# Performance work log

Measured on AMD Instinct MI355X. Metric: run time of the kernel, lower is better.

The kernel has to match this reference:

```python
import math
import jax, jax.numpy as jnp
import numpy as np

NQ, NK = 4096, 8192
D_Q, D_K, D_ATTN, H, D_OUT = 256, 256, 64, 4, 256


def setup_inputs() -> dict:
    key = jax.random.key(0)
    ks = jax.random.split(key, 10)
    s = 0.02
    return {
        "x_Q": jax.random.normal(ks[0], (NQ, D_Q), jnp.float32),
        "x_K": jax.random.normal(ks[1], (NK, D_K), jnp.float32),
        "mask": jax.random.randint(ks[2], (NQ, NK), 0, 2, jnp.int32),
        # per-head projection weights, stored as (H, in, out) so y = x @ W
        "Wq": jax.random.normal(ks[3], (H, D_Q, D_ATTN), jnp.float32) * s,
        "Wk": jax.random.normal(ks[4], (H, D_K, D_ATTN), jnp.float32) * s,
        "Wv": jax.random.normal(ks[5], (H, D_K, D_ATTN), jnp.float32) * s,
        # per-head gate: Linear(d_Q, 1) + sigmoid
        "Wg": jax.random.normal(ks[6], (H, D_Q), jnp.float32) * s,
        "bg": jax.random.normal(ks[7], (H,), jnp.float32) * s,
        # output projection Linear(d_attn, d_out) with bias
        "Wo": jax.random.normal(ks[8], (D_ATTN, D_OUT), jnp.float32) * s,
        "bo": jax.random.normal(ks[9], (D_OUT,), jnp.float32) * s,
    }


def reference(x_Q, x_K, mask, Wq, Wk, Wv, Wg, bg, Wo, bo):
    m = mask.astype(x_Q.dtype)  # (NQ, NK) 0/1
    # Stacked per-head projections (original loops over heads)
    Q = jnp.einsum("nq,hqa->hna", x_Q, Wq)  # (H, NQ, A)
    K = jnp.einsum("mk,hka->hma", x_K, Wk)  # (H, NK, A)
    V = jnp.einsum("mk,hka->hma", x_K, Wv)  # (H, NK, A)
    scale = 1.0 / math.sqrt(D_ATTN)
    scores = jnp.einsum("hna,hma->hnm", Q, K) * scale  # (H, NQ, NK)
    # masked_softmax: (mask * x).masked_fill(mask == 0, -inf) then softmax over keys
    X = jnp.where(m == 0, -jnp.inf, m * scores)
    attn = jax.nn.softmax(X, axis=-1)
    heads = jnp.einsum("hnm,hma->hna", attn, V)  # (H, NQ, A)
    gates = jax.nn.sigmoid(jnp.einsum("nq,hq->hn", x_Q, Wg) + bg[:, None])  # (H, NQ)
    combined = jnp.einsum("hna,hn->na", heads, gates)  # (NQ, A)
    return combined @ Wo + bo  # (NQ, D_OUT)
```

## Files before the change

### kernel.cpp

```cpp
#include <hip/hip_runtime.h>
#include <hip/hip_bf16.h>

#define NQ 4096
#define NK 8192
#define DQK 256
#define DA 64
#define NH 4
#define DOUT 256
#define KSPLIT 16
#define KLEN (NK / KSPLIT)
#define NQT (NQ / 32)
#define LOG2E 1.44269504088896340736f
#define QSCALE (0.125f * LOG2E)

typedef __attribute__((ext_vector_type(8))) short bf16x8;
typedef __attribute__((ext_vector_type(4))) float f32x4;
typedef __attribute__((ext_vector_type(4))) _Float16 f16x4;

__device__ inline unsigned short f2bf(float f) {
  union { float f; unsigned u; } v; v.f = f;
  unsigned r = v.u + 0x7fff + ((v.u >> 16) & 1);
  return (unsigned short)(r >> 16);
}

__device__ inline unsigned pk2(float a, float b) {
  float2 t; t.x = a; t.y = b;
  __hip_bfloat162 r = __float22bfloat162_rn(t);
  return *(unsigned*)&r;
}

__global__ __launch_bounds__(256) void maskbits_kernel(
    const int* __restrict__ mask, unsigned long long* __restrict__ bits64) {
  const int NW = 8192 * 4;
  int wid = blockIdx.x * 4 + (threadIdx.x >> 6);
  int lane = threadIdx.x & 63;
  for (int j = 0; j < 2; ++j) {
    int v[8];
#pragma unroll
    for (int u = 0; u < 8; ++u) {
      int c = wid + (j * 8 + u) * NW;
      v[u] = mask[(size_t)(c >> 7) * NK + (c & 127) * 64 + lane];
    }
#pragma unroll
    for (int u = 0; u < 8; ++u) {
      unsigned long long b = __ballot(v[u] != 0);
      int c = wid + (j * 8 + u) * NW;
      if (lane == 0) bits64[c] = b;
    }
  }
}

__global__ __launch_bounds__(256) void proj_kernel(
    const float* __restrict__ xQ, const float* __restrict__ xK,
    const float* __restrict__ Wq, const float* __restrict__ Wk,
    const float* __restrict__ Wv,
    unsigned short* __restrict__ Qp, unsigned short* __restrict__ Kp,
    unsigned short* __restrict__ Vt) {
  __shared__ __align__(16) unsigned short Wt[64][264];

  int b = blockIdx.x;
  int proj, h, rb;
  if (b < 64)        { proj = 0; h = b >> 4;  rb = b & 15; }
  else if (b < 192)  { proj = 1; b -= 64;  h = b >> 5; rb = b & 31; }
  else               { proj = 2; b -= 192; h = b >> 5; rb = b & 31; }
  const float* x = (proj == 0) ? xQ : xK;
  const float* W = (proj == 0 ? Wq : (proj == 1 ? Wk : Wv)) + (size_t)h * 256 * 64;

  for (int i = threadIdx.x; i < 16384; i += 256)
    Wt[i & 63][i >> 6] = f2bf(W[i]);
  __syncthreads();

  int lane = threadIdx.x & 63, wv = threadIdx.x >> 6;
  int quad = lane >> 4, n16 = lane & 15;
  int r0 = rb * 256 + wv * 64;

  f32x4 acc[4][4];
#pragma unroll
  for (int mt = 0; mt < 4; ++mt)
#pragma unroll
    for (int nt = 0; nt < 4; ++nt)
      acc[mt][nt] = (f32x4){0.f, 0.f, 0.f, 0.f};

#pragma unroll
  for (int it = 0; it < 8; ++it) {
    const int k0 = it * 32;
    bf16x8 af[4];
#pragma unroll
    for (int mt = 0; mt < 4; ++mt) {
      const float* xp = x + (size_t)(r0 + mt * 16 + n16) * 256 + k0 + quad * 8;
      const float4 a0 = *(const float4*)xp;
      const float4 a1 = *(const float4*)(xp + 4);
      bf16x8 a;
      a[0] = (short)f2bf(a0.x); a[1] = (short)f2bf(a0.y);
      a[2] = (short)f2bf(a0.z); a[3] = (short)f2bf(a0.w);
      a[4] = (short)f2bf(a1.x); a[5] = (short)f2bf(a1.y);
      a[6] = (short)f2bf(a1.z); a[7] = (short)f2bf(a1.w);
      af[mt] = a;
    }
    bf16x8 bfr[4];
#pragma unroll
    for (int nt = 0; nt < 4; ++nt)
      bfr[nt] = *(const bf16x8*)&Wt[nt * 16 + n16][k0 + quad * 8];
#pragma unroll
    for (int mt = 0; mt < 4; ++mt)
#pragma unroll
      for (int nt = 0; nt < 4; ++nt)
        acc[mt][nt] = __builtin_amdgcn_mfma_f32_16x16x32_bf16(
            af[mt], bfr[nt], acc[mt][nt], 0, 0, 0);
  }

  if (proj < 2) {
    unsigned short* outp =
        (proj == 0 ? Qp : Kp) + (size_t)h * (size_t)(proj == 0 ? NQ : NK) * 64;
    const float sc = (proj == 0) ? QSCALE : 1.0f;
#pragma unroll
    for (int mt = 0; mt < 4; ++mt)
#pragma unroll
      for (int nt = 0; nt < 4; ++nt)
#pragma unroll
        for (int r = 0; r < 4; ++r) {
          int row = r0 + mt * 16 + quad * 4 + r;
          int col = nt * 16 + n16;
          outp[(size_t)row * 64 + col] = f2bf(acc[mt][nt][r] * sc);
        }
  } else {
    unsigned short* vtp = Vt + (size_t)h * 64 * NK;
#pragma unroll
    for (int mt = 0; mt < 4; ++mt)
#pragma unroll
      for (int nt = 0; nt < 4; ++nt) {
        int d = nt * 16 + n16;
        int key0 = r0 + mt * 16 + quad * 4;
        ushort4 pk;
        pk.x = f2bf(acc[mt][nt][0]); pk.y = f2bf(acc[mt][nt][1]);
        pk.z = f2bf(acc[mt][nt][2]); pk.w = f2bf(acc[mt][nt][3]);
        *(ushort4*)&vtp[(size_t)d * NK + key0] = pk;
      }
  }
}

__global__ __launch_bounds__(256) void attn_kernel(
    const unsigned short* __restrict__ Qp, const unsigned short* __restrict__ Kp,
    const unsigned short* __restrict__ Vt, const unsigned* __restrict__ bits,
    _Float16* __restrict__ Opart, float* __restrict__ Lpart) {
  __shared__ __align__(16) unsigned short Plds[4][2][32][40];

  int b = blockIdx.x;
  int ks = b & 15, h = (b >> 4) & 3, qg = b >> 6;
  int wv = threadIdx.x >> 6, lane = threadIdx.x & 63;
  int quad = lane >> 4, n16 = lane & 15;
  int qt = qg * 4 + wv;
  int qb = qt * 32;

  bf16x8 qf[2][2];
#pragma unroll
  for (int qc = 0; qc < 2; ++qc)
#pragma unroll
    for (int c = 0; c < 2; ++c)
      qf[qc][c] = *(const bf16x8*)&Qp[((size_t)h * NQ + qb + qc * 16 + n16) * 64 +
                                      c * 32 + quad * 8];

  bf16x8 onesA;
  {
    short v = (n16 == 0) ? (short)0x3F80 : (short)0;
#pragma unroll
    for (int i = 0; i < 8; ++i) onesA[i] = v;
  }

  f32x4 o[4][2];
#pragma unroll
  for (int dt = 0; dt < 4; ++dt)
#pragma unroll
    for (int qc = 0; qc < 2; ++qc) o[dt][qc] = (f32x4){0.f, 0.f, 0.f, 0.f};
  f32x4 l5[2];
  l5[0] = (f32x4){0.f, 0.f, 0.f, 0.f};
  l5[1] = (f32x4){0.f, 0.f, 0.f, 0.f};

  const unsigned short* Kptr =
      Kp + (size_t)h * NK * 64 + (size_t)(ks * KLEN + n16) * 64 + quad * 8;
  const unsigned short* Vptr =
      Vt + (size_t)h * 64 * NK + (size_t)n16 * NK + ks * KLEN + quad * 8;
  const unsigned* bq0 = bits + (size_t)(qb + n16) * (NK / 32) + ks * (KLEN / 32);
  const unsigned* bq1 = bits + (size_t)(qb + 16 + n16) * (NK / 32) + ks * (KLEN / 32);

  bf16x8 kf[2][2], vf[4];
#pragma unroll
  for (int kr = 0; kr < 2; ++kr)
#pragma unroll
    for (int c = 0; c < 2; ++c)
      kf[kr][c] = *(const bf16x8*)(Kptr + kr * 16 * 64 + c * 32);
#pragma unroll
  for (int dt = 0; dt < 4; ++dt)
    vf[dt] = *(const bf16x8*)(Vptr + (size_t)dt * 16 * NK);

#pragma unroll
  for (int kb = 0; kb < KLEN / 32; ++kb) {
    bf16x8 kn[2][2], vn[4];
    if (kb < KLEN / 32 - 1) {
      const unsigned short* Kn = Kptr + (size_t)(kb + 1) * 32 * 64;
      const unsigned short* Vn = Vptr + (kb + 1) * 32;
#pragma unroll
      for (int kr = 0; kr < 2; ++kr)
#pragma unroll
        for (int c = 0; c < 2; ++c)
          kn[kr][c] = *(const bf16x8*)(Kn + kr * 16 * 64 + c * 32);
#pragma unroll
      for (int dt = 0; dt < 4; ++dt)
        vn[dt] = *(const bf16x8*)(Vn + (size_t)dt * 16 * NK);
    }
    unsigned wqa0 = bq0[kb];
    unsigned wqa1 = bq1[kb];

    f32x4 s[2][2];
#pragma unroll
    for (int kr = 0; kr < 2; ++kr)
#pragma unroll
      for (int qc = 0; qc < 2; ++qc) {
        f32x4 acc = (f32x4){0.f, 0.f, 0.f, 0.f};
        acc = __builtin_amdgcn_mfma_f32_16x16x32_bf16(kf[kr][0], qf[qc][0], acc, 0, 0, 0);
        acc = __builtin_amdgcn_mfma_f32_16x16x32_bf16(kf[kr][1], qf[qc][1], acc, 0, 0, 0);
        s[kr][qc] = acc;
      }

    unsigned short* pbuf = &Plds[wv][kb & 1][0][0];
#pragma unroll
    for (int qc = 0; qc < 2; ++qc) {
      unsigned wq0 = (qc == 0 ? wqa0 : wqa1) >> (quad * 4);
      float e[8];
#pragma unroll
      for (int kr = 0; kr < 2; ++kr)
#pragma unroll
        for (int r = 0; r < 4; ++r) {
          float ev = __builtin_amdgcn_exp2f(s[kr][qc][r]);
          e[kr * 4 + r] = (wq0 & (1u << (kr * 16 + r))) ? ev : 0.f;
        }
      unsigned short* prow = pbuf + (qc * 16 + n16) * 40;
      uint2 w01, w23;
      w01.x = pk2(e[0], e[1]); w01.y = pk2(e[2], e[3]);
      w23.x = pk2(e[4], e[5]); w23.y = pk2(e[6], e[7]);
      *(uint2*)(prow + quad * 4) = w01;
      *(uint2*)(prow + 16 + quad * 4) = w23;
    }

    bf16x8 pb0 = *(const bf16x8*)(pbuf + n16 * 40 + quad * 8);
    bf16x8 pb1 = *(const bf16x8*)(pbuf + (16 + n16) * 40 + quad * 8);

#pragma unroll
    for (int dt = 0; dt < 4; ++dt) {
      o[dt][0] = __builtin_amdgcn_mfma_f32_16x16x32_bf16(vf[dt], pb0, o[dt][0], 0, 0, 0);
      o[dt][1] = __builtin_amdgcn_mfma_f32_16x16x32_bf16(vf[dt], pb1, o[dt][1], 0, 0, 0);
    }
    l5[0] = __builtin_amdgcn_mfma_f32_16x16x32_bf16(onesA, pb0, l5[0], 0, 0, 0);
    l5[1] = __builtin_amdgcn_mfma_f32_16x16x32_bf16(onesA, pb1, l5[1], 0, 0, 0);

    if (kb < KLEN / 32 - 1) {
#pragma unroll
      for (int kr = 0; kr < 2; ++kr)
#pragma unroll
        for (int c = 0; c < 2; ++c) kf[kr][c] = kn[kr][c];
#pragma unroll
      for (int dt = 0; dt < 4; ++dt) vf[dt] = vn[dt];
    }
  }

  const size_t tb = ((size_t)h * NQT + qt) * KSPLIT + ks;
#pragma unroll
  for (int qc = 0; qc < 2; ++qc) {
#pragma unroll
    for (int dt = 0; dt < 4; ++dt) {
      size_t idx = (tb * 32 + qc * 16 + n16) * 64 + dt * 16 + quad * 4;
      f16x4 ov;
      ov[0] = (_Float16)o[dt][qc][0]; ov[1] = (_Float16)o[dt][qc][1];
      ov[2] = (_Float16)o[dt][qc][2]; ov[3] = (_Float16)o[dt][qc][3];
      *(f16x4*)&Opart[idx] = ov;
    }
  }
  if (quad == 0) {
    Lpart[tb * 32 + n16] = l5[0][0];
    Lpart[tb * 32 + 16 + n16] = l5[1][0];
  }
}

__global__ __launch_bounds__(256) void combine_kernel(
    const _Float16* __restrict__ Opart, const float* __restrict__ Lpart,
    const float* __restrict__ xQ, const float* __restrict__ Wg,
    const float* __restrict__ bg, const float* __restrict__ Wo,
    const float* __restrict__ bo, float* __restrict__ out) {
  __shared__ float comb[16][64];
  __shared__ float gred[16][4][4];
  __shared__ float glds[16][4];
  int nb = blockIdx.x;
  int tid = threadIdx.x;

  {
    int r = tid >> 4, hh = (tid >> 2) & 3, c = tid & 3;
    const float* xp = xQ + (size_t)(nb * 16 + r) * 256 + c * 64;
    const float* wp = Wg + hh * 256 + c * 64;
    float s = 0.f;
#pragma unroll
    for (int e = 0; e < 64; ++e) s = fmaf(xp[e], wp[e], s);
    gred[r][hh][c] = s;
  }
  __syncthreads();
  if (tid < 64) {
    int r = tid >> 2, hh = tid & 3;
    float s = gred[r][hh][0] + gred[r][hh][1] + gred[r][hh][2] + gred[r][hh][3];
    glds[r][hh] = 1.f / (1.f + __expf(-(s + bg[hh])));
  }
  __syncthreads();

  int r4 = tid >> 6, a = tid & 63;
  int qt = nb >> 1, rbase = (nb & 1) * 16;

  for (int p = 0; p < 4; ++p) {
    int r = p * 4 + r4;
    int rl = rbase + r;
    float csum = 0.f;
#pragma unroll
    for (int h = 0; h < NH; ++h) {
      size_t t0 = ((size_t)h * NQT + qt) * KSPLIT;
      float accO = 0.f, lt = 0.f;
#pragma unroll
      for (int s = 0; s < KSPLIT; ++s) {
        size_t t = t0 + s;
        accO += (float)Opart[(t * 32 + rl) * 64 + a];
        lt += Lpart[t * 32 + rl];
      }
      csum += glds[r][h] * accO / lt;
    }
    comb[r][a] = csum;
  }
  __syncthreads();

  int j = tid;
  float accv[16];
#pragma unroll
  for (int r = 0; r < 16; ++r) accv[r] = bo[j];
  for (int aa = 0; aa < 64; ++aa) {
    float w = Wo[(size_t)aa * 256 + j];
#pragma unroll
    for (int r = 0; r < 16; ++r) accv[r] = fmaf(comb[r][aa], w, accv[r]);
  }
#pragma unroll
  for (int r = 0; r < 16; ++r)
    out[(size_t)(nb * 16 + r) * 256 + j] = accv[r];
}

extern "C" void kernel_launch(void* const* d_in, const int* in_sizes, int n_in,
                              void* d_out, int out_size, void* d_ws, size_t ws_size,
                              hipStream_t stream) {
  const float* xQ  = (const float*)d_in[0];
  const float* xK  = (const float*)d_in[1];
  const int*   mask= (const int*)d_in[2];
  const float* Wq  = (const float*)d_in[3];
  const float* Wk  = (const float*)d_in[4];
  const float* Wv  = (const float*)d_in[5];
  const float* Wg  = (const float*)d_in[6];
  const float* bg  = (const float*)d_in[7];
  const float* Wo  = (const float*)d_in[8];
  const float* bo  = (const float*)d_in[9];
  float* out = (float*)d_out;

  char* ws = (char*)d_ws;
  unsigned short* Qp   = (unsigned short*)(ws + 0);
  unsigned short* Kp   = (unsigned short*)(ws + 2097152);
  unsigned short* Vt   = (unsigned short*)(ws + 6291456);
  unsigned*       bits = (unsigned*)(ws + 10485760);
  float*          Lp   = (float*)(ws + 14745600);
  _Float16*       Op   = (_Float16*)(ws + 15794176);

  maskbits_kernel<<<dim3(8192), dim3(256), 0, stream>>>(
      mask, (unsigned long long*)bits);
  proj_kernel<<<dim3(320), dim3(256), 0, stream>>>(xQ, xK, Wq, Wk, Wv, Qp, Kp, Vt);
  attn_kernel<<<dim3(2048), dim3(256), 0, stream>>>(Qp, Kp, Vt, bits, Op, Lp);
  combine_kernel<<<dim3(NQ / 16), dim3(256), 0, stream>>>(Op, Lp, xQ, Wg, bg,
                                                          Wo, bo, out);
}
```

Measured before the change: 429.5 us.

## Keep softmax probabilities in registers using fp16 MFMA and halve key split

```diff
diff --git a/kernel.cpp b/kernel.cpp
--- a/kernel.cpp
+++ b/kernel.cpp
@@ -7,7 +7,7 @@
 #define DA 64
 #define NH 4
 #define DOUT 256
-#define KSPLIT 16
+#define KSPLIT 8
 #define KLEN (NK / KSPLIT)
 #define NQT (NQ / 32)
 #define LOG2E 1.44269504088896340736f
@@ -21,12 +21,6 @@
   union { float f; unsigned u; } v; v.f = f;
   unsigned r = v.u + 0x7fff + ((v.u >> 16) & 1);
   return (unsigned short)(r >> 16);
-}
-
-__device__ inline unsigned pk2(float a, float b) {
-  float2 t; t.x = a; t.y = b;
-  __hip_bfloat162 r = __float22bfloat162_rn(t);
-  return *(unsigned*)&r;
 }
 
 __global__ __launch_bounds__(256) void maskbits_kernel(
@@ -55,7 +49,7 @@
     const float* __restrict__ Wq, const float* __restrict__ Wk,
     const float* __restrict__ Wv,
     unsigned short* __restrict__ Qp, unsigned short* __restrict__ Kp,
-    unsigned short* __restrict__ Vt) {
+    _Float16* __restrict__ Vt) {
   __shared__ __align__(16) unsigned short Wt[64][264];
 
   int b = blockIdx.x;
@@ -124,29 +118,27 @@
           outp[(size_t)row * 64 + col] = f2bf(acc[mt][nt][r] * sc);
         }
   } else {
-    unsigned short* vtp = Vt + (size_t)h * 64 * NK;
+    _Float16* vtp = Vt + (size_t)h * 64 * NK;
 #pragma unroll
     for (int mt = 0; mt < 4; ++mt)
 #pragma unroll
       for (int nt = 0; nt < 4; ++nt) {
         int d = nt * 16 + n16;
         int key0 = r0 + mt * 16 + quad * 4;
-        ushort4 pk;
-        pk.x = f2bf(acc[mt][nt][0]); pk.y = f2bf(acc[mt][nt][1]);
-        pk.z = f2bf(acc[mt][nt][2]); pk.w = f2bf(acc[mt][nt][3]);
-        *(ushort4*)&vtp[(size_t)d * NK + key0] = pk;
+        f16x4 pk;
+        pk[0] = (_Float16)acc[mt][nt][0]; pk[1] = (_Float16)acc[mt][nt][1];
+        pk[2] = (_Float16)acc[mt][nt][2]; pk[3] = (_Float16)acc[mt][nt][3];
+        *(f16x4*)&vtp[(size_t)d * NK + key0] = pk;
       }
   }
 }
 
 __global__ __launch_bounds__(256) void attn_kernel(
     const unsigned short* __restrict__ Qp, const unsigned short* __restrict__ Kp,
-    const unsigned short* __restrict__ Vt, const unsigned* __restrict__ bits,
+    const _Float16* __restrict__ Vt, const unsigned* __restrict__ bits,
     _Float16* __restrict__ Opart, float* __restrict__ Lpart) {
-  __shared__ __align__(16) unsigned short Plds[4][2][32][40];
-
   int b = blockIdx.x;
-  int ks = b & 15, h = (b >> 4) & 3, qg = b >> 6;
+  int ks = b & 7, h = (b >> 3) & 3, qg = b >> 5;
   int wv = threadIdx.x >> 6, lane = threadIdx.x & 63;
   int quad = lane >> 4, n16 = lane & 15;
   int qt = qg * 4 + wv;
@@ -160,56 +152,40 @@
       qf[qc][c] = *(const bf16x8*)&Qp[((size_t)h * NQ + qb + qc * 16 + n16) * 64 +
                                       c * 32 + quad * 8];
 
-  bf16x8 onesA;
-  {
-    short v = (n16 == 0) ? (short)0x3F80 : (short)0;
-#pragma unroll
-    for (int i = 0; i < 8; ++i) onesA[i] = v;
-  }
-
   f32x4 o[4][2];
 #pragma unroll
   for (int dt = 0; dt < 4; ++dt)
 #pragma unroll
     for (int qc = 0; qc < 2; ++qc) o[dt][qc] = (f32x4){0.f, 0.f, 0.f, 0.f};
-  f32x4 l5[2];
-  l5[0] = (f32x4){0.f, 0.f, 0.f, 0.f};
-  l5[1] = (f32x4){0.f, 0.f, 0.f, 0.f};
+  float ls[2] = {0.f, 0.f};
 
   const unsigned short* Kptr =
       Kp + (size_t)h * NK * 64 + (size_t)(ks * KLEN + n16) * 64 + quad * 8;
-  const unsigned short* Vptr =
-      Vt + (size_t)h * 64 * NK + (size_t)n16 * NK + ks * KLEN + quad * 8;
+  const _Float16* Vptr =
+      Vt + (size_t)h * 64 * NK + (size_t)n16 * NK + ks * KLEN + quad * 4;
   const unsigned* bq0 = bits + (size_t)(qb + n16) * (NK / 32) + ks * (KLEN / 32);
   const unsigned* bq1 = bits + (size_t)(qb + 16 + n16) * (NK / 32) + ks * (KLEN / 32);
 
-  bf16x8 kf[2][2], vf[4];
-#pragma unroll
-  for (int kr = 0; kr < 2; ++kr)
-#pragma unroll
-    for (int c = 0; c < 2; ++c)
-      kf[kr][c] = *(const bf16x8*)(Kptr + kr * 16 * 64 + c * 32);
-#pragma unroll
-  for (int dt = 0; dt < 4; ++dt)
-    vf[dt] = *(const bf16x8*)(Vptr + (size_t)dt * 16 * NK);
-
-#pragma unroll
+#pragma unroll 2
   for (int kb = 0; kb < KLEN / 32; ++kb) {
-    bf16x8 kn[2][2], vn[4];
-    if (kb < KLEN / 32 - 1) {
-      const unsigned short* Kn = Kptr + (size_t)(kb + 1) * 32 * 64;
-      const unsigned short* Vn = Vptr + (kb + 1) * 32;
-#pragma unroll
-      for (int kr = 0; kr < 2; ++kr)
-#pragma unroll
-        for (int c = 0; c < 2; ++c)
-          kn[kr][c] = *(const bf16x8*)(Kn + kr * 16 * 64 + c * 32);
-#pragma unroll
-      for (int dt = 0; dt < 4; ++dt)
-        vn[dt] = *(const bf16x8*)(Vn + (size_t)dt * 16 * NK);
-    }
     unsigned wqa0 = bq0[kb];
     unsigned wqa1 = bq1[kb];
+
+    const unsigned short* Kg = Kptr + (size_t)kb * 32 * 64;
+    bf16x8 kf[2][2];
+#pragma unroll
+    for (int kr = 0; kr < 2; ++kr)
+#pragma unroll
+      for (int c = 0; c < 2; ++c)
+        kf[kr][c] = *(const bf16x8*)(Kg + kr * 16 * 64 + c * 32);
+
+    const _Float16* Vg = Vptr + kb * 32;
+    f16x4 vf[4][2];
+#pragma unroll
+    for (int dt = 0; dt < 4; ++dt)
+#pragma unroll
+      for (int kr = 0; kr < 2; ++kr)
+        vf[dt][kr] = *(const f16x4*)(Vg + (size_t)dt * 16 * NK + kr * 16);
 
     f32x4 s[2][2];
 #pragma unroll
@@ -222,45 +198,40 @@
         s[kr][qc] = acc;
       }
 
-    unsigned short* pbuf = &Plds[wv][kb & 1][0][0];
 #pragma unroll
     for (int qc = 0; qc < 2; ++qc) {
-      unsigned wq0 = (qc == 0 ? wqa0 : wqa1) >> (quad * 4);
-      float e[8];
-#pragma unroll
-      for (int kr = 0; kr < 2; ++kr)
-#pragma unroll
-        for (int r = 0; r < 4; ++r) {
-          float ev = __builtin_amdgcn_exp2f(s[kr][qc][r]);
-          e[kr * 4 + r] = (wq0 & (1u << (kr * 16 + r))) ? ev : 0.f;
-        }
-      unsigned short* prow = pbuf + (qc * 16 + n16) * 40;
-      uint2 w01, w23;
-      w01.x = pk2(e[0], e[1]); w01.y = pk2(e[2], e[3]);
-      w23.x = pk2(e[4], e[5]); w23.y = pk2(e[6], e[7]);
-      *(uint2*)(prow + quad * 4) = w01;
-      *(uint2*)(prow + 16 + quad * 4) = w23;
-    }
-
-    bf16x8 pb0 = *(const bf16x8*)(pbuf + n16 * 40 + quad * 8);
-    bf16x8 pb1 = *(const bf16x8*)(pbuf + (16 + n16) * 40 + quad * 8);
-
-#pragma unroll
-    for (int dt = 0; dt < 4; ++dt) {
-      o[dt][0] = __builtin_amdgcn_mfma_f32_16x16x32_bf16(vf[dt], pb0, o[dt][0], 0, 0, 0);
-      o[dt][1] = __builtin_amdgcn_mfma_f32_16x16x32_bf16(vf[dt], pb1, o[dt][1], 0, 0, 0);
-    }
-    l5[0] = __builtin_amdgcn_mfma_f32_16x16x32_bf16(onesA, pb0, l5[0], 0, 0, 0);
-    l5[1] = __builtin_amdgcn_mfma_f32_16x16x32_bf16(onesA, pb1, l5[1], 0, 0, 0);
-
-    if (kb < KLEN / 32 - 1) {
-#pragma unroll
-      for (int kr = 0; kr < 2; ++kr)
-#pragma unroll
-        for (int c = 0; c < 2; ++c) kf[kr][c] = kn[kr][c];
-#pragma unroll
-      for (int dt = 0; dt < 4; ++dt) vf[dt] = vn[dt];
-    }
+      unsigned wq = (qc == 0 ? wqa0 : wqa1) >> (quad * 4);
+      f16x4 pf[2];
+#pragma unroll
+      for (int kr = 0; kr < 2; ++kr) {
+        float e0 = __builtin_amdgcn_exp2f(s[kr][qc][0]);
+        float e1 = __builtin_amdgcn_exp2f(s[kr][qc][1]);
+        float e2 = __builtin_amdgcn_exp2f(s[kr][qc][2]);
+        float e3 = __builtin_amdgcn_exp2f(s[kr][qc][3]);
+        e0 = (wq & (1u << (kr * 16 + 0))) ? e0 : 0.f;
+        e1 = (wq & (1u << (kr * 16 + 1))) ? e1 : 0.f;
+        e2 = (wq & (1u << (kr * 16 + 2))) ? e2 : 0.f;
+        e3 = (wq & (1u << (kr * 16 + 3))) ? e3 : 0.f;
+        ls[qc] += (e0 + e1) + (e2 + e3);
+        f16x4 p;
+        p[0] = (_Float16)e0; p[1] = (_Float16)e1;
+        p[2] = (_Float16)e2; p[3] = (_Float16)e3;
+        pf[kr] = p;
+      }
+#pragma unroll
+      for (int dt = 0; dt < 4; ++dt) {
+        o[dt][qc] = __builtin_amdgcn_mfma_f32_16x16x16f16(vf[dt][0], pf[0],
+                                                          o[dt][qc], 0, 0, 0);
+        o[dt][qc] = __builtin_amdgcn_mfma_f32_16x16x16f16(vf[dt][1], pf[1],
+                                                          o[dt][qc], 0, 0, 0);
+      }
+    }
+  }
+
+#pragma unroll
+  for (int qc = 0; qc < 2; ++qc) {
+    ls[qc] += __shfl_xor(ls[qc], 16);
+    ls[qc] += __shfl_xor(ls[qc], 32);
   }
 
   const size_t tb = ((size_t)h * NQT + qt) * KSPLIT + ks;
@@ -276,8 +247,8 @@
     }
   }
   if (quad == 0) {
-    Lpart[tb * 32 + n16] = l5[0][0];
-    Lpart[tb * 32 + 16 + n16] = l5[1][0];
+    Lpart[tb * 32 + n16] = ls[0];
+    Lpart[tb * 32 + 16 + n16] = ls[1];
   }
 }
 
@@ -364,7 +335,7 @@
   char* ws = (char*)d_ws;
   unsigned short* Qp   = (unsigned short*)(ws + 0);
   unsigned short* Kp   = (unsigned short*)(ws + 2097152);
-  unsigned short* Vt   = (unsigned short*)(ws + 6291456);
+  _Float16*       Vt   = (_Float16*)(ws + 6291456);
   unsigned*       bits = (unsigned*)(ws + 10485760);
   float*          Lp   = (float*)(ws + 14745600);
   _Float16*       Op   = (_Float16*)(ws + 15794176);
@@ -372,7 +343,7 @@
   maskbits_kernel<<<dim3(8192), dim3(256), 0, stream>>>(
       mask, (unsigned long long*)bits);
   proj_kernel<<<dim3(320), dim3(256), 0, stream>>>(xQ, xK, Wq, Wk, Wv, Qp, Kp, Vt);
-  attn_kernel<<<dim3(2048), dim3(256), 0, stream>>>(Qp, Kp, Vt, bits, Op, Lp);
+  attn_kernel<<<dim3(1024), dim3(256), 0, stream>>>(Qp, Kp, Vt, bits, Op, Lp);
   combine_kernel<<<dim3(NQ / 16), dim3(256), 0, stream>>>(Op, Lp, xQ, Wg, bg,
                                                           Wo, bo, out);
 }
```

Result: slower. 460.3 us (+7.2%).
